# Optimization experiments

Measured on AMD Instinct MI355X. Metric: run time of the kernel, lower is better.

## Reference

```python
import jax, jax.numpy as jnp
import numpy as np

D = 256      # channels / model dim
HEADS = 8
DK = 32
DV = 32
B, H, W = 8, 32, 32
EPS = 1e-5


def setup_inputs() -> dict:
    key = jax.random.key(0)
    ks = jax.random.split(key, 9)
    s = 0.02
    return {
        "x":  jax.random.normal(ks[0], (B, D, H, W), dtype=jnp.float32),
        "Wq": jax.random.normal(ks[1], (HEADS * DK, D), dtype=jnp.float32) * s,
        "bq": jnp.zeros((HEADS * DK,), dtype=jnp.float32),
        "Wk": jax.random.normal(ks[2], (HEADS * DK, D), dtype=jnp.float32) * s,
        "bk": jnp.zeros((HEADS * DK,), dtype=jnp.float32),
        "Wv": jax.random.normal(ks[3], (HEADS * DV, D), dtype=jnp.float32) * s,
        "bv": jnp.zeros((HEADS * DV,), dtype=jnp.float32),
        "Wo": jax.random.normal(ks[4], (D, HEADS * DK), dtype=jnp.float32) * s,
        "bo": jnp.zeros((D,), dtype=jnp.float32),
    }


def reference(x, Wq, bq, Wk, bk, Wv, bv, Wo, bo):
    b, c, h, w = x.shape
    n = h * w
    # LayerNorm over [c, h, w] per sample, no affine (functional.layer_norm default)
    mu = jnp.mean(x, axis=(1, 2, 3), keepdims=True)
    var = jnp.var(x, axis=(1, 2, 3), keepdims=True)
    xn = (x - mu) * jax.lax.rsqrt(var + EPS)
    xr = xn.reshape(b, c, n).transpose(0, 2, 1)  # [b, n, c]

    def proj(Wt, bt, dh):
        y = xr @ Wt.T + bt                        # [b, n, heads*dh]
        return y.reshape(b, n, HEADS, dh).transpose(0, 2, 1, 3)  # [b, heads, n, dh]

    q = proj(Wq, bq, DK)
    k = proj(Wk, bk, DK)
    v = proj(Wv, bv, DV)

    scores = jnp.einsum('bhid,bhjd->bhij', q, k) * (DK ** -0.5)  # [b, heads, n, n]
    att = jax.nn.softmax(scores, axis=-1)
    tmp = jnp.einsum('bhij,bhjd->bhid', att, v)                  # [b, heads, n, dv]
    tmp = tmp.transpose(0, 2, 1, 3).reshape(b, n, HEADS * DV)    # [b, n, heads*dv]
    out = tmp @ Wo.T + bo                                        # [b, n, d]
    # NOTE: original does a raw .view(b, d, h, w) WITHOUT permuting — faithful reshape
    out = out.reshape(b, c, h, w)
    return out + x
```

## Files before the change

kernel.cpp:

```cpp
#include <hip/hip_runtime.h>
#include <stdint.h>

typedef unsigned short u16;
typedef unsigned int u32;
typedef __attribute__((ext_vector_type(8))) short bf16x8;
typedef __attribute__((ext_vector_type(4))) float f32x4;
typedef __attribute__((ext_vector_type(16))) float f32x16;

#define NTOK 1024
#define DMODEL 256
#define NHEAD 8
#define DK 32
#define NBATCH 8
#define PER_B (DMODEL * NTOK)

__device__ __forceinline__ float b2f(u16 h) {
    union { unsigned u; float f; } c; c.u = ((unsigned)h) << 16; return c.f;
}
__device__ __forceinline__ u16 f2b(float f) {
    unsigned u = __float_as_uint(f);
    unsigned r = u + 0x7fffu + ((u >> 16) & 1u);
    return (u16)(r >> 16);
}

__global__ void prep(const float* __restrict__ Wq, const float* __restrict__ Wk,
                     const float* __restrict__ Wv, const float* __restrict__ Wo,
                     u16* __restrict__ wb,
                     const float* __restrict__ x, float* __restrict__ part) {
    int bx = blockIdx.x;
    int t = threadIdx.x;
    if (bx < 256) {
        int m = bx >> 6;
        const float* W = (m == 0) ? Wq : (m == 1) ? Wk : (m == 2) ? Wv : Wo;
        int i = ((bx & 63) * 256 + t) * 4;
        float4 v = *(const float4*)&W[i];
        ushort4 o;
        o.x = f2b(v.x); o.y = f2b(v.y); o.z = f2b(v.z); o.w = f2b(v.w);
        *(ushort4*)&wb[m * 65536 + i] = o;
        return;
    }
    int blk = bx - 256;
    int b = blk >> 3, sl = blk & 7;
    int w = t >> 6, l = t & 63;
    const float* xb = x + (size_t)b * PER_B + sl * (PER_B / 8);
    float s = 0.f, ss = 0.f;
    for (int base = 0; base < PER_B / 8; base += 1024) {
        float4 v = *(const float4*)&xb[base + t * 4];
        s += v.x + v.y + v.z + v.w;
        ss += v.x * v.x + v.y * v.y + v.z * v.z + v.w * v.w;
    }
    for (int d = 1; d < 64; d <<= 1) {
        s += __shfl_xor(s, d, 64);
        ss += __shfl_xor(ss, d, 64);
    }
    __shared__ float red[2][4];
    if (l == 0) { red[0][w] = s; red[1][w] = ss; }
    __syncthreads();
    if (t == 0) {
        float S = red[0][0] + red[0][1] + red[0][2] + red[0][3];
        float SS = red[1][0] + red[1][1] + red[1][2] + red[1][3];
        part[(b * 8 + sl) * 2] = S;
        part[(b * 8 + sl) * 2 + 1] = SS;
    }
}

__global__ void normT(const float* __restrict__ x, const float* __restrict__ part,
                      u16* __restrict__ xn) {
    int b = blockIdx.z;
    int n0 = blockIdx.x * 32;
    int c0 = blockIdx.y * 32;
    int tx = threadIdx.x, ty = threadIdx.y;
    __shared__ float s_mu, s_rs;
    __shared__ float tile[32][33];
    if (tx == 0 && ty == 0) {
        float S = 0.f, SS = 0.f;
        for (int i = 0; i < 8; ++i) { S += part[(b * 8 + i) * 2]; SS += part[(b * 8 + i) * 2 + 1]; }
        float mu = S / (float)PER_B;
        float var = SS / (float)PER_B - mu * mu;
        s_mu = mu;
        s_rs = rsqrtf(var + 1e-5f);
    }
    __syncthreads();
    float mu = s_mu, rs = s_rs;
    const float* xb = x + (size_t)b * PER_B;
#pragma unroll
    for (int i = 0; i < 4; ++i) {
        int c = c0 + ty + i * 8;
        tile[ty + i * 8][tx] = (xb[c * NTOK + n0 + tx] - mu) * rs;
    }
    __syncthreads();
    u16* xnb = xn + (size_t)b * PER_B;
#pragma unroll
    for (int i = 0; i < 4; ++i) {
        int n = n0 + ty + i * 8;
        xnb[n * DMODEL + c0 + tx] = f2b(tile[tx][ty + i * 8]);
    }
}

__global__ __launch_bounds__(256) void qkv_gemm(
    const u16* __restrict__ xn, const u16* __restrict__ wb,
    const float* __restrict__ bq, const float* __restrict__ bk,
    const float* __restrict__ bv,
    u16* __restrict__ qo, u16* __restrict__ ko, u16* __restrict__ vo) {
    int mt = blockIdx.x;
    int ot = blockIdx.y;
    int b = blockIdx.z;
    int sel = ot >> 2;
    int o0 = (ot & 3) * 64;
    const u16* W = wb + sel * 65536;
    const float* bias = (sel == 0) ? bq : (sel == 1) ? bk : bv;

    __shared__ u16 As[64][40];
    __shared__ u16 Bs[64][40];
    int t = threadIdx.x;
    int w = t >> 6, l = t & 63;
    int lr = t >> 2;
    int lc = (t & 3) * 8;
    int qd = l >> 4, ln = l & 15;

    const u16* xb = xn + ((size_t)b * NTOK + mt * 64) * DMODEL;
    f32x4 acc[4] = {};
    for (int kb = 0; kb < 8; ++kb) {
        *(uint4*)&As[lr][lc] = *(const uint4*)&xb[lr * DMODEL + kb * 32 + lc];
        *(uint4*)&Bs[lr][lc] = *(const uint4*)&W[(o0 + lr) * DMODEL + kb * 32 + lc];
        __syncthreads();
        bf16x8 af = *(const bf16x8*)&As[w * 16 + ln][qd * 8];
#pragma unroll
        for (int ns = 0; ns < 4; ++ns) {
            bf16x8 bf = *(const bf16x8*)&Bs[ns * 16 + ln][qd * 8];
            acc[ns] = __builtin_amdgcn_mfma_f32_16x16x32_bf16(af, bf, acc[ns], 0, 0, 0);
        }
        __syncthreads();
    }
    if (sel < 2) {
        u16* outp = (sel == 0) ? qo : ko;
        float scale = (sel == 0) ? 0.25505654344884634f : 1.0f;
#pragma unroll
        for (int ns = 0; ns < 4; ++ns) {
            int o = o0 + ns * 16 + ln;
            float bias_f = bias[o];
            int head = o >> 5, d = o & 31;
#pragma unroll
            for (int r = 0; r < 4; ++r) {
                int n_row = mt * 64 + w * 16 + qd * 4 + r;
                float v = (acc[ns][r] + bias_f) * scale;
                outp[(((size_t)b * NHEAD + head) * NTOK + n_row) * DK + d] = f2b(v);
            }
        }
    } else {
        int n0 = mt * 64 + w * 16 + qd * 4;
#pragma unroll
        for (int ns = 0; ns < 4; ++ns) {
            int o = o0 + ns * 16 + ln;
            float bias_f = bias[o];
            int head = o >> 5, d = o & 31;
            ushort4 pk;
            pk.x = f2b(acc[ns][0] + bias_f);
            pk.y = f2b(acc[ns][1] + bias_f);
            pk.z = f2b(acc[ns][2] + bias_f);
            pk.w = f2b(acc[ns][3] + bias_f);
            *(ushort4*)&vo[(((size_t)b * NHEAD + head) * DK + d) * NTOK + n0] = pk;
        }
    }
}

__global__ __launch_bounds__(256, 4) void attn(
    const u16* __restrict__ qws, const u16* __restrict__ kws,
    const u16* __restrict__ vtws, u16* __restrict__ tmp) {
    int bh = blockIdx.x;
    int qp = blockIdx.y;
    int b = bh >> 3, h = bh & 7;
    const u16* Q  = qws  + (size_t)bh * NTOK * DK;
    const u16* K  = kws  + (size_t)bh * NTOK * DK;
    const u16* Vt = vtws + (size_t)bh * DK * NTOK;

    __shared__ float xl[2][64];
    __shared__ float xo[2][64][17];

    int t = threadIdx.x;
    int w = t >> 6, l = t & 63;
    int qsub = w >> 1, khalf = w & 1;
    int l31 = l & 31, hi = l >> 5;
    int kperm = (l31 & 19) | ((l31 & 4) << 1) | ((l31 & 8) >> 1);

    int q0 = qp * 64 + qsub * 32;
    int kb0 = khalf * 512;

    bf16x8 qf0 = *(const bf16x8*)&Q[(q0 + l31) * DK + hi * 8];
    bf16x8 qf1 = *(const bf16x8*)&Q[(q0 + l31) * DK + 16 + hi * 8];

    const u16* kp = K + (size_t)(kb0 + kperm) * DK + hi * 8;
    const u16* vp = Vt + (size_t)l31 * NTOK + kb0 + hi * 8;

    f32x16 oacc = {};
    float lsum = 0.f;

    bf16x8 kf0 = *(const bf16x8*)&kp[0];
    bf16x8 kf1 = *(const bf16x8*)&kp[16];
    bf16x8 va  = *(const bf16x8*)&vp[0];
    bf16x8 vb  = *(const bf16x8*)&vp[16];

#pragma unroll
    for (int kt = 0; kt < 16; ++kt) {
        bf16x8 nk0, nk1, nva, nvb;
        if (kt < 15) {
            const u16* kn = kp + (kt + 1) * 32 * DK;
            const u16* vn = vp + (kt + 1) * 32;
            nk0 = *(const bf16x8*)&kn[0];
            nk1 = *(const bf16x8*)&kn[16];
            nva = *(const bf16x8*)&vn[0];
            nvb = *(const bf16x8*)&vn[16];
        }
        f32x16 s = {};
        s = __builtin_amdgcn_mfma_f32_32x32x16_bf16(kf0, qf0, s, 0, 0, 0);
        s = __builtin_amdgcn_mfma_f32_32x32x16_bf16(kf1, qf1, s, 0, 0, 0);

        union { u32 u[4]; bf16x8 v; } pa, pb;
        float ps = 0.f;
#pragma unroll
        for (int j = 0; j < 4; ++j) {
            float e0 = __builtin_amdgcn_exp2f(s[2 * j]);
            float e1 = __builtin_amdgcn_exp2f(s[2 * j + 1]);
            float e2 = __builtin_amdgcn_exp2f(s[2 * j + 8]);
            float e3 = __builtin_amdgcn_exp2f(s[2 * j + 9]);
            ps += (e0 + e1) + (e2 + e3);
            pa.u[j] = __builtin_amdgcn_perm(__float_as_uint(e1), __float_as_uint(e0), 0x07060302u);
            pb.u[j] = __builtin_amdgcn_perm(__float_as_uint(e3), __float_as_uint(e2), 0x07060302u);
        }
        lsum += ps;

        oacc = __builtin_amdgcn_mfma_f32_32x32x16_bf16(va, pa.v, oacc, 0, 0, 0);
        oacc = __builtin_amdgcn_mfma_f32_32x32x16_bf16(vb, pb.v, oacc, 0, 0, 0);

        kf0 = nk0; kf1 = nk1; va = nva; vb = nvb;
    }

    if (khalf == 1) {
        xl[qsub][l] = lsum;
#pragma unroll
        for (int r = 0; r < 16; ++r) xo[qsub][l][r] = oacc[r];
    }
    __syncthreads();
    if (khalf == 0) {
        lsum += xl[qsub][l];
#pragma unroll
        for (int r = 0; r < 16; ++r) oacc[r] += xo[qsub][l][r];
        lsum += __shfl_xor(lsum, 32, 64);
        float linv = 1.0f / lsum;
        int qg = q0 + l31;
        u16* op = tmp + ((size_t)b * NTOK + qg) * DMODEL + h * DK;
#pragma unroll
        for (int g = 0; g < 4; ++g) {
            ushort4 pk;
            pk.x = f2b(oacc[g * 4 + 0] * linv);
            pk.y = f2b(oacc[g * 4 + 1] * linv);
            pk.z = f2b(oacc[g * 4 + 2] * linv);
            pk.w = f2b(oacc[g * 4 + 3] * linv);
            *(ushort4*)&op[g * 8 + hi * 4] = pk;
        }
    }
}

__global__ __launch_bounds__(256) void oproj(
    const u16* __restrict__ tmp, const u16* __restrict__ wb,
    const float* __restrict__ bo, const float* __restrict__ x,
    float* __restrict__ out) {
    int mt = blockIdx.x;
    int ot = blockIdx.y;
    int b = blockIdx.z;
    const u16* Wo = wb + 3 * 65536;

    __shared__ u16 As[64][40];
    __shared__ u16 Bs[64][40];
    int t = threadIdx.x;
    int w = t >> 6, l = t & 63;
    int lr = t >> 2;
    int lc = (t & 3) * 8;
    int qd = l >> 4, ln = l & 15;

    const u16* ab = tmp + ((size_t)b * NTOK + mt * 64) * DMODEL;
    f32x4 acc[4] = {};
    for (int kb = 0; kb < 8; ++kb) {
        *(uint4*)&As[lr][lc] = *(const uint4*)&ab[lr * DMODEL + kb * 32 + lc];
        *(uint4*)&Bs[lr][lc] = *(const uint4*)&Wo[(ot * 64 + lr) * DMODEL + kb * 32 + lc];
        __syncthreads();
        bf16x8 af = *(const bf16x8*)&As[w * 16 + ln][qd * 8];
#pragma unroll
        for (int ns = 0; ns < 4; ++ns) {
            bf16x8 bf = *(const bf16x8*)&Bs[ns * 16 + ln][qd * 8];
            acc[ns] = __builtin_amdgcn_mfma_f32_16x16x32_bf16(af, bf, acc[ns], 0, 0, 0);
        }
        __syncthreads();
    }
    const float* xb = x + (size_t)b * PER_B;
    float* ob = out + (size_t)b * PER_B;
#pragma unroll
    for (int ns = 0; ns < 4; ++ns) {
        int o = ot * 64 + ns * 16 + ln;
        float bias_f = bo[o];
#pragma unroll
        for (int r = 0; r < 4; ++r) {
            int n_row = mt * 64 + w * 16 + qd * 4 + r;
            size_t idx = (size_t)n_row * DMODEL + o;
            ob[idx] = acc[ns][r] + bias_f + xb[idx];
        }
    }
}

extern "C" void kernel_launch(void* const* d_in, const int* in_sizes, int n_in,
                              void* d_out, int out_size, void* d_ws, size_t ws_size,
                              hipStream_t stream) {
    const float* x  = (const float*)d_in[0];
    const float* Wq = (const float*)d_in[1];
    const float* bq = (const float*)d_in[2];
    const float* Wk = (const float*)d_in[3];
    const float* bk = (const float*)d_in[4];
    const float* Wv = (const float*)d_in[5];
    const float* bv = (const float*)d_in[6];
    const float* Wo = (const float*)d_in[7];
    const float* bo = (const float*)d_in[8];
    float* out = (float*)d_out;

    char* ws = (char*)d_ws;
    float* part = (float*)ws;
    u16* wb  = (u16*)(ws + 1024);
    u16* xn  = (u16*)(ws + 1024 + (512u << 10));
    u16* qws = (u16*)(ws + 1024 + (512u << 10) + (4u << 20));
    u16* kws = (u16*)(ws + 1024 + (512u << 10) + (8u << 20));
    u16* vws = (u16*)(ws + 1024 + (512u << 10) + (12u << 20));
    u16* tmp = xn;

    hipLaunchKernelGGL(prep, dim3(320), dim3(256), 0, stream, Wq, Wk, Wv, Wo, wb, x, part);
    hipLaunchKernelGGL(normT, dim3(32, 8, 8), dim3(32, 8), 0, stream, x, part, xn);
    hipLaunchKernelGGL(qkv_gemm, dim3(16, 12, 8), dim3(256), 0, stream,
                       xn, wb, bq, bk, bv, qws, kws, vws);
    hipLaunchKernelGGL(attn, dim3(64, 16), dim3(256), 0, stream, qws, kws, vws, tmp);
    hipLaunchKernelGGL(oproj, dim3(16, 4, 8), dim3(256), 0, stream, tmp, wb, bo, x, out);
}
```

Measured before the change: 125.9 us.

## Load GEMM fragments directly from global memory, dropping LDS staging and barriers

In the QKV projection and output projection GEMMs, each wave now loads its MFMA A and B fragments straight from global memory instead of staging 64x32 tiles through shared memory with two barriers per k-step. The k-loop is fully unrolled and launch bounds request 4 blocks per SM, so all loads can be issued early and more blocks can be resident. The cost is that every wave in a block re-reads the same weight rows from global memory, with more total global/L2 traffic and per-lane 16-byte loads that are strided by row.

Measured after the change: 150.3 us. 19.4% more time.

```diff
diff --git a/kernel.cpp b/kernel.cpp
--- a/kernel.cpp
+++ b/kernel.cpp
@@ -97,7 +97,7 @@
     }
 }
 
-__global__ __launch_bounds__(256) void qkv_gemm(
+__global__ __launch_bounds__(256, 4) void qkv_gemm(
     const u16* __restrict__ xn, const u16* __restrict__ wb,
     const float* __restrict__ bq, const float* __restrict__ bk,
     const float* __restrict__ bv,
@@ -110,27 +110,22 @@
     const u16* W = wb + sel * 65536;
     const float* bias = (sel == 0) ? bq : (sel == 1) ? bk : bv;
 
-    __shared__ u16 As[64][40];
-    __shared__ u16 Bs[64][40];
     int t = threadIdx.x;
     int w = t >> 6, l = t & 63;
-    int lr = t >> 2;
-    int lc = (t & 3) * 8;
     int qd = l >> 4, ln = l & 15;
 
-    const u16* xb = xn + ((size_t)b * NTOK + mt * 64) * DMODEL;
+    const u16* ap = xn + ((size_t)b * NTOK + mt * 64 + w * 16 + ln) * DMODEL + qd * 8;
+    const u16* wp = W + (size_t)(o0 + ln) * DMODEL + qd * 8;
+
     f32x4 acc[4] = {};
+#pragma unroll
     for (int kb = 0; kb < 8; ++kb) {
-        *(uint4*)&As[lr][lc] = *(const uint4*)&xb[lr * DMODEL + kb * 32 + lc];
-        *(uint4*)&Bs[lr][lc] = *(const uint4*)&W[(o0 + lr) * DMODEL + kb * 32 + lc];
-        __syncthreads();
-        bf16x8 af = *(const bf16x8*)&As[w * 16 + ln][qd * 8];
+        bf16x8 af = *(const bf16x8*)&ap[kb * 32];
 #pragma unroll
         for (int ns = 0; ns < 4; ++ns) {
-            bf16x8 bf = *(const bf16x8*)&Bs[ns * 16 + ln][qd * 8];
+            bf16x8 bf = *(const bf16x8*)&wp[ns * 16 * DMODEL + kb * 32];
             acc[ns] = __builtin_amdgcn_mfma_f32_16x16x32_bf16(af, bf, acc[ns], 0, 0, 0);
         }
-        __syncthreads();
     }
     if (sel < 2) {
         u16* outp = (sel == 0) ? qo : ko;
@@ -261,7 +256,7 @@
     }
 }
 
-__global__ __launch_bounds__(256) void oproj(
+__global__ __launch_bounds__(256, 4) void oproj(
     const u16* __restrict__ tmp, const u16* __restrict__ wb,
     const float* __restrict__ bo, const float* __restrict__ x,
     float* __restrict__ out) {
@@ -270,27 +265,22 @@
     int b = blockIdx.z;
     const u16* Wo = wb + 3 * 65536;
 
-    __shared__ u16 As[64][40];
-    __shared__ u16 Bs[64][40];
     int t = threadIdx.x;
     int w = t >> 6, l = t & 63;
-    int lr = t >> 2;
-    int lc = (t & 3) * 8;
     int qd = l >> 4, ln = l & 15;
 
-    const u16* ab = tmp + ((size_t)b * NTOK + mt * 64) * DMODEL;
+    const u16* ap = tmp + ((size_t)b * NTOK + mt * 64 + w * 16 + ln) * DMODEL + qd * 8;
+    const u16* wp = Wo + (size_t)(ot * 64 + ln) * DMODEL + qd * 8;
+
     f32x4 acc[4] = {};
+#pragma unroll
     for (int kb = 0; kb < 8; ++kb) {
-        *(uint4*)&As[lr][lc] = *(const uint4*)&ab[lr * DMODEL + kb * 32 + lc];
-        *(uint4*)&Bs[lr][lc] = *(const uint4*)&Wo[(ot * 64 + lr) * DMODEL + kb * 32 + lc];
-        __syncthreads();
-        bf16x8 af = *(const bf16x8*)&As[w * 16 + ln][qd * 8];
+        bf16x8 af = *(const bf16x8*)&ap[kb * 32];
 #pragma unroll
         for (int ns = 0; ns < 4; ++ns) {
-            bf16x8 bf = *(const bf16x8*)&Bs[ns * 16 + ln][qd * 8];
+            bf16x8 bf = *(const bf16x8*)&wp[ns * 16 * DMODEL + kb * 32];
             acc[ns] = __builtin_amdgcn_mfma_f32_16x16x32_bf16(af, bf, acc[ns], 0, 0, 0);
         }
-        __syncthreads();
     }
     const float* xb = x + (size_t)b * PER_B;
     float* ob = out + (size_t)b * PER_B;
```
